# Performance work log

Hardware: AMD Instinct MI355X
Metric: run time of the kernel (lower is better)

## Reference

```python
import jax, jax.numpy as jnp
import numpy as np

N, IN_DIM, OUT_DIM = 8192, 256, 64
NEG_BIG = -9e15
LRELU_SLOPE = 0.01  # torch F.leaky_relu default


def setup_inputs() -> dict:
    key = jax.random.key(0)
    k1, k2, k3, k4 = jax.random.split(key, 4)
    inp = jax.random.normal(k1, (N, IN_DIM), dtype=jnp.float32)
    adj = jax.random.randint(k2, (N, N), 0, 2, dtype=jnp.int32)
    # xavier_uniform with gain=1.414
    limW = 1.414 * np.sqrt(6.0 / (IN_DIM + OUT_DIM))
    W = jax.random.uniform(k3, (IN_DIM, OUT_DIM), minval=-limW, maxval=limW, dtype=jnp.float32)
    lima = 1.414 * np.sqrt(6.0 / (2 * OUT_DIM + 1))
    a = jax.random.uniform(k4, (2 * OUT_DIM, 1), minval=-lima, maxval=lima, dtype=jnp.float32)
    return {"input": inp, "adj": adj, "W": W, "a": a}


def reference(input, adj, W, a):
    h = input @ W                      # [N, D]
    a1, a2 = a[:OUT_DIM, 0], a[OUT_DIM:, 0]
    # e[i,j] = leaky_relu(a1.h_i + a2.h_j) == the concat-based score, no NxNx2D tensor
    f1 = h @ a1                        # [N]
    f2 = h @ a2                        # [N]
    e = jax.nn.leaky_relu(f1[:, None] + f2[None, :], negative_slope=LRELU_SLOPE)  # [N, N]
    face_Rhand = e[1, 2]
    face_Lhand = e[1, 3]
    Rhand_Lhand = e[3, 2]
    attention = jnp.where(adj > 0, e, jnp.float32(NEG_BIG))
    alpha = jax.nn.softmax(attention, axis=1)
    h_prime = alpha @ h                # [N, D]
    return (h_prime, face_Rhand, face_Lhand, Rhand_Lhand)
```

## Files before the change

### kernel.cpp

```cpp
#include <hip/hip_runtime.h>
#include <hip/hip_bf16.h>

#define GN 8192
#define KD 256
#define OD 64
#define LOG2E 1.44269504f
#define INV_LOG2E 0.69314718f

typedef __attribute__((ext_vector_type(8))) short bf16x8;
typedef __attribute__((ext_vector_type(4))) float f32x4;

__device__ __forceinline__ short f2bf(float x) {
  __hip_bfloat16 b = __float2bfloat16(x);
  return *reinterpret_cast<short*>(&b);
}

__global__ __launch_bounds__(256) void gat_k1(
    const float* __restrict__ input, const float* __restrict__ W,
    const float* __restrict__ a, __hip_bfloat16* __restrict__ hT,
    float* __restrict__ f1p, float* __restrict__ f2p, float* __restrict__ out)
{
  __shared__ float Wl[KD * OD];
  __shared__ float inT[KD * 33];
  __shared__ float red1[8][32];
  __shared__ float red2[8][32];
  __shared__ float s1row[32];
  __shared__ float s2row[32];

  const int tid = threadIdx.x;
  const int i0 = blockIdx.x * 32;

  for (int idx = tid; idx < KD * OD / 4; idx += 256)
    ((float4*)Wl)[idx] = ((const float4*)W)[idx];

#pragma unroll
  for (int it = 0; it < 8; ++it) {
    int idx = tid + it * 256;
    int r = idx >> 6, k4 = idx & 63;
    float4 v = *(const float4*)(input + (long)(i0 + r) * KD + k4 * 4);
    inT[(k4 * 4 + 0) * 33 + r] = v.x;
    inT[(k4 * 4 + 1) * 33 + r] = v.y;
    inT[(k4 * 4 + 2) * 33 + r] = v.z;
    inT[(k4 * 4 + 3) * 33 + r] = v.w;
  }
  __syncthreads();

  const int r = tid & 31;
  const int cg = tid >> 5;
  float acc[8];
#pragma unroll
  for (int c = 0; c < 8; ++c) acc[c] = 0.f;

#pragma unroll 4
  for (int k = 0; k < KD; ++k) {
    float inv = inT[k * 33 + r];
    float4 wa = *(const float4*)&Wl[k * 64 + cg * 8];
    float4 wb = *(const float4*)&Wl[k * 64 + cg * 8 + 4];
    acc[0] += inv * wa.x; acc[1] += inv * wa.y;
    acc[2] += inv * wa.z; acc[3] += inv * wa.w;
    acc[4] += inv * wb.x; acc[5] += inv * wb.y;
    acc[6] += inv * wb.z; acc[7] += inv * wb.w;
  }

#pragma unroll
  for (int c = 0; c < 8; ++c)
    hT[(long)(cg * 8 + c) * GN + i0 + r] = __float2bfloat16(acc[c]);

  float s1 = 0.f, s2 = 0.f;
#pragma unroll
  for (int c = 0; c < 8; ++c) {
    s1 += acc[c] * a[cg * 8 + c];
    s2 += acc[c] * a[OD + cg * 8 + c];
  }
  red1[cg][r] = s1; red2[cg][r] = s2;
  __syncthreads();
  if (tid < 32) {
    float f1 = 0.f, f2 = 0.f;
#pragma unroll
    for (int g = 0; g < 8; ++g) { f1 += red1[g][tid]; f2 += red2[g][tid]; }
    s1row[tid] = f1; s2row[tid] = f2;
    f1p[i0 + tid] = f1 * LOG2E;
    f2p[i0 + tid] = f2 * LOG2E;
  }
  __syncthreads();
  if (blockIdx.x == 0 && tid == 0) {
    float e12 = s1row[1] + s2row[2];
    float e13 = s1row[1] + s2row[3];
    float e32 = s1row[3] + s2row[2];
    out[(long)GN * OD + 0] = fmaxf(e12, 0.01f * e12);
    out[(long)GN * OD + 1] = fmaxf(e13, 0.01f * e13);
    out[(long)GN * OD + 2] = fmaxf(e32, 0.01f * e32);
  }
}

__global__ __launch_bounds__(512, 4) void gat_k2(
    const int* __restrict__ adj, const __hip_bfloat16* __restrict__ hT,
    const float* __restrict__ f1p, const float* __restrict__ f2p,
    float* __restrict__ out)
{
  __shared__ float pbuf[8][16][66];
  __shared__ float sbuf[8][16];

  const int tid = threadIdx.x;
  const int lane = tid & 63;
  const int wv = tid >> 6;
  const int tn = lane & 15;
  const int quad = lane >> 4;
  const int i0 = blockIdx.x * 16;
  const int jbase = wv * 1024;

  const float f1r = f1p[i0 + tn];

  f32x4 acc[4];
#pragma unroll
  for (int nf = 0; nf < 4; ++nf) acc[nf] = (f32x4){0.f, 0.f, 0.f, 0.f};
  f32x4 accS = (f32x4){0.f, 0.f, 0.f, 0.f};

  bf16x8 ones;
  {
    short ov = (tn == 0) ? (short)0x3F80 : (short)0;
#pragma unroll
    for (int i = 0; i < 8; ++i) ones[i] = ov;
  }

  const int* ap = adj + (long)(i0 + tn) * GN + jbase + quad * 8;
  const float* fp = f2p + jbase + quad * 8;
  const __hip_bfloat16* hp = hT + jbase + quad * 8 + tn * (long)GN;

  int4 a0 = *(const int4*)ap;
  int4 a1 = *(const int4*)(ap + 4);
  float4 F0 = *(const float4*)fp;
  float4 F1 = *(const float4*)(fp + 4);

  for (int c = 0; c < 32; ++c) {
    int4 ca0 = a0, ca1 = a1;
    float4 cF0 = F0, cF1 = F1;
    if (c + 1 < 32) {
      a0 = *(const int4*)(ap + (c + 1) * 32);
      a1 = *(const int4*)(ap + (c + 1) * 32 + 4);
      F0 = *(const float4*)(fp + (c + 1) * 32);
      F1 = *(const float4*)(fp + (c + 1) * 32 + 4);
    }
    bf16x8 b0 = *(const bf16x8*)(hp + c * 32 + 0 * 16 * (long)GN);
    bf16x8 b1 = *(const bf16x8*)(hp + c * 32 + 1 * 16 * (long)GN);
    bf16x8 b2 = *(const bf16x8*)(hp + c * 32 + 2 * 16 * (long)GN);
    bf16x8 b3 = *(const bf16x8*)(hp + c * 32 + 3 * 16 * (long)GN);

    union { bf16x8 v; short s[8]; } wf;
    {
      float e0 = f1r + cF0.x, e1 = f1r + cF0.y, e2 = f1r + cF0.z, e3 = f1r + cF0.w;
      float e4 = f1r + cF1.x, e5 = f1r + cF1.y, e6 = f1r + cF1.z, e7 = f1r + cF1.w;
      float w0 = (ca0.x > 0) ? exp2f(fmaxf(e0, 0.01f * e0)) : 0.f;
      float w1 = (ca0.y > 0) ? exp2f(fmaxf(e1, 0.01f * e1)) : 0.f;
      float w2 = (ca0.z > 0) ? exp2f(fmaxf(e2, 0.01f * e2)) : 0.f;
      float w3 = (ca0.w > 0) ? exp2f(fmaxf(e3, 0.01f * e3)) : 0.f;
      float w4 = (ca1.x > 0) ? exp2f(fmaxf(e4, 0.01f * e4)) : 0.f;
      float w5 = (ca1.y > 0) ? exp2f(fmaxf(e5, 0.01f * e5)) : 0.f;
      float w6 = (ca1.z > 0) ? exp2f(fmaxf(e6, 0.01f * e6)) : 0.f;
      float w7 = (ca1.w > 0) ? exp2f(fmaxf(e7, 0.01f * e7)) : 0.f;
      wf.s[0] = f2bf(w0); wf.s[1] = f2bf(w1); wf.s[2] = f2bf(w2); wf.s[3] = f2bf(w3);
      wf.s[4] = f2bf(w4); wf.s[5] = f2bf(w5); wf.s[6] = f2bf(w6); wf.s[7] = f2bf(w7);
    }

    acc[0] = __builtin_amdgcn_mfma_f32_16x16x32_bf16(wf.v, b0, acc[0], 0, 0, 0);
    acc[1] = __builtin_amdgcn_mfma_f32_16x16x32_bf16(wf.v, b1, acc[1], 0, 0, 0);
    acc[2] = __builtin_amdgcn_mfma_f32_16x16x32_bf16(wf.v, b2, acc[2], 0, 0, 0);
    acc[3] = __builtin_amdgcn_mfma_f32_16x16x32_bf16(wf.v, b3, acc[3], 0, 0, 0);
    accS   = __builtin_amdgcn_mfma_f32_16x16x32_bf16(wf.v, ones, accS, 0, 0, 0);
  }

#pragma unroll
  for (int nf = 0; nf < 4; ++nf)
#pragma unroll
    for (int rg = 0; rg < 4; ++rg)
      pbuf[wv][quad * 4 + rg][nf * 16 + tn] = acc[nf][rg];
  if (tn == 0) {
#pragma unroll
    for (int rg = 0; rg < 4; ++rg)
      sbuf[wv][quad * 4 + rg] = accS[rg];
  }
  __syncthreads();
  for (int t = tid; t < 16 * OD; t += 512) {
    int rr = t >> 6, cc = t & 63;
    float num = 0.f, den = 0.f;
#pragma unroll
    for (int w = 0; w < 8; ++w) { num += pbuf[w][rr][cc]; den += sbuf[w][rr]; }
    out[(long)(i0 + rr) * OD + cc] = num / den;
  }
}

extern "C" void kernel_launch(void* const* d_in, const int* in_sizes, int n_in,
                              void* d_out, int out_size, void* d_ws, size_t ws_size,
                              hipStream_t stream) {
  const float* input = (const float*)d_in[0];
  const int* adj     = (const int*)d_in[1];
  const float* W     = (const float*)d_in[2];
  const float* a     = (const float*)d_in[3];
  float* out = (float*)d_out;

  __hip_bfloat16* hT = (__hip_bfloat16*)d_ws;
  float* f1p = (float*)((char*)d_ws + (size_t)OD * GN * sizeof(__hip_bfloat16));
  float* f2p = f1p + GN;

  gat_k1<<<256, 256, 0, stream>>>(input, W, a, hT, f1p, f2p, out);
  gat_k2<<<512, 512, 0, stream>>>(adj, hT, f1p, f2p, out);
}
```

Measured before the change: 447.2 us.

## Deepen load pipelining in attention kernel and stage f2 in LDS

The aggregation kernel now runs 4 waves per block, each covering 2048 columns. Each wave keeps four slices of adjacency and hT loads in flight, with sched_barrier fences so the compiler keeps the loads ahead of the MFMA work. The f2 scores are copied into LDS once per block, and that LDS buffer is reused for the final cross-wave reduction. The per-element math is cheaper: exp2 uses the raw builtin, masked entries use exp2(-256) instead of a branch, and bf16 packing truncates via byte perm instead of rounding. In exchange, fewer waves are resident per CU and the weights lose a little precision from truncation.

```diff
diff --git a/kernel.cpp b/kernel.cpp
--- a/kernel.cpp
+++ b/kernel.cpp
@@ -5,15 +5,23 @@
 #define KD 256
 #define OD 64
 #define LOG2E 1.44269504f
-#define INV_LOG2E 0.69314718f
 
 typedef __attribute__((ext_vector_type(8))) short bf16x8;
 typedef __attribute__((ext_vector_type(4))) float f32x4;
 
-__device__ __forceinline__ short f2bf(float x) {
-  __hip_bfloat16 b = __float2bfloat16(x);
-  return *reinterpret_cast<short*>(&b);
-}
+__device__ __forceinline__ float fexp2(float x) {
+#if __has_builtin(__builtin_amdgcn_exp2f)
+  return __builtin_amdgcn_exp2f(x);
+#else
+  return exp2f(x);
+#endif
+}
+
+#if __has_builtin(__builtin_amdgcn_sched_barrier)
+#define SCHED_FENCE() __builtin_amdgcn_sched_barrier(0)
+#else
+#define SCHED_FENCE()
+#endif
 
 __global__ __launch_bounds__(256) void gat_k1(
     const float* __restrict__ input, const float* __restrict__ W,
@@ -93,13 +101,15 @@
   }
 }
 
-__global__ __launch_bounds__(512, 4) void gat_k2(
+struct Asl { int4 a0, a1; };
+struct Bsl { bf16x8 b0, b1, b2, b3; };
+
+__global__ __launch_bounds__(256, 2) void gat_k2(
     const int* __restrict__ adj, const __hip_bfloat16* __restrict__ hT,
     const float* __restrict__ f1p, const float* __restrict__ f2p,
     float* __restrict__ out)
 {
-  __shared__ float pbuf[8][16][66];
-  __shared__ float sbuf[8][16];
+  __shared__ float f2l[GN];
 
   const int tid = threadIdx.x;
   const int lane = tid & 63;
@@ -107,9 +117,17 @@
   const int tn = lane & 15;
   const int quad = lane >> 4;
   const int i0 = blockIdx.x * 16;
-  const int jbase = wv * 1024;
+  const int jq = wv * 2048;
+
+  for (int i = tid; i < GN / 4; i += 256)
+    ((float4*)f2l)[i] = ((const float4*)f2p)[i];
 
   const float f1r = f1p[i0 + tn];
+  __syncthreads();
+
+  const int* ap = adj + (long)(i0 + tn) * GN + jq + quad * 8;
+  const __hip_bfloat16* hp = hT + (long)tn * GN + jq + quad * 8;
+  const float* f2q = f2l + jq + quad * 8;
 
   f32x4 acc[4];
 #pragma unroll
@@ -123,68 +141,96 @@
     for (int i = 0; i < 8; ++i) ones[i] = ov;
   }
 
-  const int* ap = adj + (long)(i0 + tn) * GN + jbase + quad * 8;
-  const float* fp = f2p + jbase + quad * 8;
-  const __hip_bfloat16* hp = hT + jbase + quad * 8 + tn * (long)GN;
-
-  int4 a0 = *(const int4*)ap;
-  int4 a1 = *(const int4*)(ap + 4);
-  float4 F0 = *(const float4*)fp;
-  float4 F1 = *(const float4*)(fp + 4);
-
-  for (int c = 0; c < 32; ++c) {
-    int4 ca0 = a0, ca1 = a1;
-    float4 cF0 = F0, cF1 = F1;
-    if (c + 1 < 32) {
-      a0 = *(const int4*)(ap + (c + 1) * 32);
-      a1 = *(const int4*)(ap + (c + 1) * 32 + 4);
-      F0 = *(const float4*)(fp + (c + 1) * 32);
-      F1 = *(const float4*)(fp + (c + 1) * 32 + 4);
-    }
-    bf16x8 b0 = *(const bf16x8*)(hp + c * 32 + 0 * 16 * (long)GN);
-    bf16x8 b1 = *(const bf16x8*)(hp + c * 32 + 1 * 16 * (long)GN);
-    bf16x8 b2 = *(const bf16x8*)(hp + c * 32 + 2 * 16 * (long)GN);
-    bf16x8 b3 = *(const bf16x8*)(hp + c * 32 + 3 * 16 * (long)GN);
-
-    union { bf16x8 v; short s[8]; } wf;
-    {
-      float e0 = f1r + cF0.x, e1 = f1r + cF0.y, e2 = f1r + cF0.z, e3 = f1r + cF0.w;
-      float e4 = f1r + cF1.x, e5 = f1r + cF1.y, e6 = f1r + cF1.z, e7 = f1r + cF1.w;
-      float w0 = (ca0.x > 0) ? exp2f(fmaxf(e0, 0.01f * e0)) : 0.f;
-      float w1 = (ca0.y > 0) ? exp2f(fmaxf(e1, 0.01f * e1)) : 0.f;
-      float w2 = (ca0.z > 0) ? exp2f(fmaxf(e2, 0.01f * e2)) : 0.f;
-      float w3 = (ca0.w > 0) ? exp2f(fmaxf(e3, 0.01f * e3)) : 0.f;
-      float w4 = (ca1.x > 0) ? exp2f(fmaxf(e4, 0.01f * e4)) : 0.f;
-      float w5 = (ca1.y > 0) ? exp2f(fmaxf(e5, 0.01f * e5)) : 0.f;
-      float w6 = (ca1.z > 0) ? exp2f(fmaxf(e6, 0.01f * e6)) : 0.f;
-      float w7 = (ca1.w > 0) ? exp2f(fmaxf(e7, 0.01f * e7)) : 0.f;
-      wf.s[0] = f2bf(w0); wf.s[1] = f2bf(w1); wf.s[2] = f2bf(w2); wf.s[3] = f2bf(w3);
-      wf.s[4] = f2bf(w4); wf.s[5] = f2bf(w5); wf.s[6] = f2bf(w6); wf.s[7] = f2bf(w7);
-    }
-
-    acc[0] = __builtin_amdgcn_mfma_f32_16x16x32_bf16(wf.v, b0, acc[0], 0, 0, 0);
-    acc[1] = __builtin_amdgcn_mfma_f32_16x16x32_bf16(wf.v, b1, acc[1], 0, 0, 0);
-    acc[2] = __builtin_amdgcn_mfma_f32_16x16x32_bf16(wf.v, b2, acc[2], 0, 0, 0);
-    acc[3] = __builtin_amdgcn_mfma_f32_16x16x32_bf16(wf.v, b3, acc[3], 0, 0, 0);
-    accS   = __builtin_amdgcn_mfma_f32_16x16x32_bf16(wf.v, ones, accS, 0, 0, 0);
-  }
-
+  auto loadA = [&](int s) {
+    Asl r;
+    r.a0 = *(const int4*)(ap + s * 32);
+    r.a1 = *(const int4*)(ap + s * 32 + 4);
+    return r;
+  };
+  auto loadB = [&](int s) {
+    Bsl r;
+    r.b0 = *(const bf16x8*)(hp + 0 * 16 * (long)GN + s * 32);
+    r.b1 = *(const bf16x8*)(hp + 1 * 16 * (long)GN + s * 32);
+    r.b2 = *(const bf16x8*)(hp + 2 * 16 * (long)GN + s * 32);
+    r.b3 = *(const bf16x8*)(hp + 3 * 16 * (long)GN + s * 32);
+    return r;
+  };
+  auto computeSlice = [&](int s, const Asl& ca, const Bsl& cb) {
+    const float4 f20 = *(const float4*)(f2q + s * 32);
+    const float4 f21 = *(const float4*)(f2q + s * 32 + 4);
+    float e0 = f1r + f20.x, e1 = f1r + f20.y, e2 = f1r + f20.z, e3 = f1r + f20.w;
+    float e4 = f1r + f21.x, e5 = f1r + f21.y, e6 = f1r + f21.z, e7 = f1r + f21.w;
+    float v0 = fexp2((ca.a0.x > 0) ? fmaxf(e0, 0.01f * e0) : -256.f);
+    float v1 = fexp2((ca.a0.y > 0) ? fmaxf(e1, 0.01f * e1) : -256.f);
+    float v2 = fexp2((ca.a0.z > 0) ? fmaxf(e2, 0.01f * e2) : -256.f);
+    float v3 = fexp2((ca.a0.w > 0) ? fmaxf(e3, 0.01f * e3) : -256.f);
+    float v4 = fexp2((ca.a1.x > 0) ? fmaxf(e4, 0.01f * e4) : -256.f);
+    float v5 = fexp2((ca.a1.y > 0) ? fmaxf(e5, 0.01f * e5) : -256.f);
+    float v6 = fexp2((ca.a1.z > 0) ? fmaxf(e6, 0.01f * e6) : -256.f);
+    float v7 = fexp2((ca.a1.w > 0) ? fmaxf(e7, 0.01f * e7) : -256.f);
+    union { bf16x8 v; unsigned u[4]; } wf;
+    wf.u[0] = __builtin_amdgcn_perm(__float_as_uint(v1), __float_as_uint(v0), 0x07060302u);
+    wf.u[1] = __builtin_amdgcn_perm(__float_as_uint(v3), __float_as_uint(v2), 0x07060302u);
+    wf.u[2] = __builtin_amdgcn_perm(__float_as_uint(v5), __float_as_uint(v4), 0x07060302u);
+    wf.u[3] = __builtin_amdgcn_perm(__float_as_uint(v7), __float_as_uint(v6), 0x07060302u);
+    acc[0] = __builtin_amdgcn_mfma_f32_16x16x32_bf16(wf.v, cb.b0, acc[0], 0, 0, 0);
+    acc[1] = __builtin_amdgcn_mfma_f32_16x16x32_bf16(wf.v, cb.b1, acc[1], 0, 0, 0);
+    acc[2] = __builtin_amdgcn_mfma_f32_16x16x32_bf16(wf.v, cb.b2, acc[2], 0, 0, 0);
+    acc[3] = __builtin_amdgcn_mfma_f32_16x16x32_bf16(wf.v, cb.b3, acc[3], 0, 0, 0);
+    accS   = __builtin_amdgcn_mfma_f32_16x16x32_bf16(wf.v, ones,  accS,   0, 0, 0);
+  };
+
+  Asl A0 = loadA(0), A1 = loadA(1), A2 = loadA(2), A3 = loadA(3);
+  Bsl B0 = loadB(0), B1 = loadB(1), B2 = loadB(2), B3 = loadB(3);
+  SCHED_FENCE();
+
+  for (int t = 0; t < 16; ++t) {
+    const int s = t * 4;
+    {
+      Asl ca = A0; Bsl cb = B0;
+      if (s + 4 < 64) { A0 = loadA(s + 4); B0 = loadB(s + 4); }
+      SCHED_FENCE();
+      computeSlice(s, ca, cb);
+    }
+    {
+      Asl ca = A1; Bsl cb = B1;
+      if (s + 5 < 64) { A1 = loadA(s + 5); B1 = loadB(s + 5); }
+      SCHED_FENCE();
+      computeSlice(s + 1, ca, cb);
+    }
+    {
+      Asl ca = A2; Bsl cb = B2;
+      if (s + 6 < 64) { A2 = loadA(s + 6); B2 = loadB(s + 6); }
+      SCHED_FENCE();
+      computeSlice(s + 2, ca, cb);
+    }
+    {
+      Asl ca = A3; Bsl cb = B3;
+      if (s + 7 < 64) { A3 = loadA(s + 7); B3 = loadB(s + 7); }
+      SCHED_FENCE();
+      computeSlice(s + 3, ca, cb);
+    }
+  }
+
+  __syncthreads();
+  float* pb = f2l;
+  float* sb = f2l + 4 * 16 * 68;
 #pragma unroll
   for (int nf = 0; nf < 4; ++nf)
 #pragma unroll
-    for (int rg = 0; rg < 4; ++rg)
-      pbuf[wv][quad * 4 + rg][nf * 16 + tn] = acc[nf][rg];
+    for (int rgi = 0; rgi < 4; ++rgi)
+      pb[(wv * 16 + quad * 4 + rgi) * 68 + nf * 16 + tn] = acc[nf][rgi];
   if (tn == 0) {
 #pragma unroll
-    for (int rg = 0; rg < 4; ++rg)
-      sbuf[wv][quad * 4 + rg] = accS[rg];
-  }
-  __syncthreads();
-  for (int t = tid; t < 16 * OD; t += 512) {
+    for (int rgi = 0; rgi < 4; ++rgi)
+      sb[wv * 16 + quad * 4 + rgi] = accS[rgi];
+  }
+  __syncthreads();
+  for (int t = tid; t < 16 * OD; t += 256) {
     int rr = t >> 6, cc = t & 63;
-    float num = 0.f, den = 0.f;
-#pragma unroll
-    for (int w = 0; w < 8; ++w) { num += pbuf[w][rr][cc]; den += sbuf[w][rr]; }
+    float num = pb[(0 * 16 + rr) * 68 + cc] + pb[(1 * 16 + rr) * 68 + cc] +
+                pb[(2 * 16 + rr) * 68 + cc] + pb[(3 * 16 + rr) * 68 + cc];
+    float den = sb[0 * 16 + rr] + sb[1 * 16 + rr] + sb[2 * 16 + rr] + sb[3 * 16 + rr];
     out[(long)(i0 + rr) * OD + cc] = num / den;
   }
 }
@@ -198,10 +244,11 @@
   const float* a     = (const float*)d_in[3];
   float* out = (float*)d_out;
 
-  __hip_bfloat16* hT = (__hip_bfloat16*)d_ws;
-  float* f1p = (float*)((char*)d_ws + (size_t)OD * GN * sizeof(__hip_bfloat16));
+  char* ws = (char*)d_ws;
+  __hip_bfloat16* hT = (__hip_bfloat16*)ws;
+  float* f1p = (float*)(ws + (size_t)OD * GN * 2);
   float* f2p = f1p + GN;
 
   gat_k1<<<256, 256, 0, stream>>>(input, W, a, hT, f1p, f2p, out);
-  gat_k2<<<512, 512, 0, stream>>>(adj, hT, f1p, f2p, out);
-}
+  gat_k2<<<512, 256, 0, stream>>>(adj, hT, f1p, f2p, out);
+}
```

Result: faster. 425.2 us (-4.9%).
